# Performance work log

Hardware: AMD Instinct MI355X
Metric: run time of the kernel (lower is better)

## Reference

```python
import jax, jax.numpy as jnp
import numpy as np
import math

B, T, L, M = 2, 16, 256, 512
D, H, DH, HT, ROT = 1024, 16, 64, 8, 32
EPS = 1e-5
NEG = jnp.float32(-1e9)
SCALE = 1.0 / math.sqrt(DH)


def _ln(x, g, b):
    mu = jnp.mean(x, -1, keepdims=True)
    var = jnp.mean((x - mu) ** 2, -1, keepdims=True)
    return (x - mu) * jax.lax.rsqrt(var + EPS) * g + b


def _rotate_half(x):
    x1, x2 = jnp.split(x, 2, axis=-1)
    return jnp.concatenate([-x2, x1], axis=-1)


def _apply_rope(t, pos):
    # t: (..., DH), pos broadcastable to (..., ROT)
    t_rot, t_pass = t[..., :ROT], t[..., ROT:]
    t_rot = t_rot * jnp.cos(pos) + _rotate_half(t_rot) * jnp.sin(pos)
    return jnp.concatenate([t_rot, t_pass], axis=-1)


def _decoder_layer(x, context, rope,
                   ca_ng, ca_nb, ca_cng, ca_cnb, ca_wq, ca_wkv, ca_wo,
                   ta_ng, ta_nb, ta_wqkv, ta_bqkv, ta_wo,
                   ff_ng, ff_nb, ff_w1, ff_w2,
                   context_mask, attn_mask):
    # ---- CrossAttention over flattened (t l) sequence ----
    xf = x.reshape(B, T * L, D)
    xn = _ln(xf, ca_ng, ca_nb)
    cn = _ln(context, ca_cng, ca_cnb)
    q = (xn @ ca_wq).reshape(B, T * L, H, DH)
    k, v = jnp.split(cn @ ca_wkv, 2, axis=-1)
    k = k.reshape(B, M, H, DH)
    v = v.reshape(B, M, H, DH)
    scores = jnp.einsum('bnhd,bmhd->bhnm', q, k) * SCALE
    scores = jnp.where(context_mask[:, None, None, :], scores, NEG)
    attn = jax.nn.softmax(scores, axis=-1)
    o = jnp.einsum('bhnm,bmhd->bnhd', attn, v).reshape(B, T * L, H * DH)
    x = x + (o @ ca_wo).reshape(B, T, L, D)

    # ---- PatchWiseTemporalAttention: attention over T at each spatial l ----
    xn = _ln(x, ta_ng, ta_nb)
    qkv = xn @ ta_wqkv + ta_bqkv  # (B,T,L,3*HT*DH)
    q, k, v = jnp.split(qkv, 3, axis=-1)
    q = q.reshape(B, T, L, HT, DH)
    k = k.reshape(B, T, L, HT, DH)
    v = v.reshape(B, T, L, HT, DH)
    # varlen rotary: masks are left-aligned so packed position == frame index t
    pos = rope[:, None, None, :]  # (T,1,1,ROT)
    q = _apply_rope(q, pos)
    k = _apply_rope(k, pos)
    scores = jnp.einsum('bqlhd,bklhd->blhqk', q, k) * SCALE
    scores = jnp.where(attn_mask[:, None, None, None, :], scores, NEG)
    attn = jax.nn.softmax(scores, axis=-1)
    o = jnp.einsum('blhqk,bklhd->bqlhd', attn, v).reshape(B, T, L, HT * DH)
    # pad_input fills zeros at invalid (masked) query rows before to_out (no bias)
    o = o * attn_mask[:, :, None, None].astype(o.dtype)
    x = x + o @ ta_wo

    # ---- FeedForward (LN -> Linear -> GELU(exact) -> Linear) ----
    h = jax.nn.gelu(_ln(x, ff_ng, ff_nb) @ ff_w1, approximate=False)
    x = x + h @ ff_w2
    return x


def setup_inputs():
    key = jax.random.key(0)
    ks = jax.random.split(key, 16)
    s = 0.02
    inner, inner_t, hid = H * DH, HT * DH, 4 * D
    lens = jax.random.randint(ks[0], (B,), 2, T + 1)
    attn_mask = jnp.arange(T)[None, :] < lens[:, None]  # left-aligned ragged lengths
    clens = jax.random.randint(ks[1], (B,), M // 2, M + 1)
    context_mask = jnp.arange(M)[None, :] < clens[:, None]
    return dict(
        x=jax.random.normal(ks[2], (B, T, L, D), jnp.float32),
        context=jax.random.normal(ks[3], (B, M, D), jnp.float32),
        rope=jax.random.normal(ks[4], (T, ROT), jnp.float32),
        ca_ng=jnp.ones((D,), jnp.float32), ca_nb=jnp.zeros((D,), jnp.float32),
        ca_cng=jnp.ones((D,), jnp.float32), ca_cnb=jnp.zeros((D,), jnp.float32),
        ca_wq=jax.random.normal(ks[5], (D, inner), jnp.float32) * s,
        ca_wkv=jax.random.normal(ks[6], (D, 2 * inner), jnp.float32) * s,
        ca_wo=jax.random.normal(ks[7], (inner, D), jnp.float32) * s,
        ta_ng=jnp.ones((D,), jnp.float32), ta_nb=jnp.zeros((D,), jnp.float32),
        ta_wqkv=jax.random.normal(ks[8], (D, 3 * inner_t), jnp.float32) * s,
        ta_bqkv=jnp.zeros((3 * inner_t,), jnp.float32),
        ta_wo=jax.random.normal(ks[9], (inner_t, D), jnp.float32) * s,
        ff_ng=jnp.ones((D,), jnp.float32), ff_nb=jnp.zeros((D,), jnp.float32),
        ff_w1=jax.random.normal(ks[10], (D, hid), jnp.float32) * s,
        ff_w2=jax.random.normal(ks[11], (hid, D), jnp.float32) * s,
        context_mask=context_mask,
        attn_mask=attn_mask,
    )


def reference(x, context, rope,
              ca_ng, ca_nb, ca_cng, ca_cnb, ca_wq, ca_wkv, ca_wo,
              ta_ng, ta_nb, ta_wqkv, ta_bqkv, ta_wo,
              ff_ng, ff_nb, ff_w1, ff_w2,
              context_mask, attn_mask):
    return _decoder_layer(x, context, rope,
                          ca_ng, ca_nb, ca_cng, ca_cnb, ca_wq, ca_wkv, ca_wo,
                          ta_ng, ta_nb, ta_wqkv, ta_bqkv, ta_wo,
                          ff_ng, ff_nb, ff_w1, ff_w2,
                          context_mask, attn_mask)
```

## Files before the change

kernel.cpp:

```cpp
#include <hip/hip_runtime.h>
#include <hip/hip_bf16.h>
#include <stdint.h>

#define DEV static __device__ __forceinline__

constexpr int kB = 2, kT = 16, kL = 256, kM = 512;
constexpr int kD = 1024, kH = 16, kDH = 64, kHT = 8, kROT = 32;
constexpr int kN = kT * kL;
constexpr float kEPS = 1e-5f;
constexpr float kNEG = -1.0e9f;
constexpr float kSCALE = 0.125f;

typedef __attribute__((ext_vector_type(8))) short short8;
typedef __attribute__((ext_vector_type(4))) float floatx4;
typedef __attribute__((ext_vector_type(16))) float floatx16;

DEV float b2f(__hip_bfloat16 v) { return __bfloat162float(v); }
DEV __hip_bfloat16 f2b(float v) { return __float2bfloat16(v); }
DEV float s2f(short x) {
  __hip_bfloat16_raw r; r.x = (unsigned short)x;
  return __bfloat162float(__hip_bfloat16(r));
}

DEV void gl2lds16(const __hip_bfloat16* g, __hip_bfloat16* l) {
  __builtin_amdgcn_global_load_lds(
      (const __attribute__((address_space(1))) void*)g,
      (__attribute__((address_space(3))) void*)l, 16, 0, 0);
}

struct TransArgs {
  const float* src[7];
  __hip_bfloat16* dst[7];
  const unsigned char* cmraw;
  const unsigned char* amraw;
  int* cmask;
  int* amask;
};
__constant__ const int kTKd[7] = {1024, 1024, 1024, 1024, 512, 1024, 4096};
__constant__ const int kTNd[7] = {1024, 2048, 1024, 1536, 1024, 4096, 1024};
__constant__ const int kTCum[8] = {0, 1024, 3072, 4096, 5632, 6144, 10240, 14336};

DEV int mask_val(const unsigned char* raw, int i) {
  unsigned char b1 = raw[1], b3 = raw[3];
  if (b1 == 0x3F) return ((const unsigned short*)raw)[i] != 0;
  if (b3 == 0x3F) return ((const float*)raw)[i] != 0.0f;
  if (b1 == 1)    return raw[i] != 0;
  return ((const int*)raw)[i] != 0;
}

__global__ __launch_bounds__(256) void transpose_all(TransArgs a) {
  int id = blockIdx.x;
  if (id >= 14336) {
    if (id == 14336) {
      for (int i = threadIdx.x; i < kB * kM; i += 256)
        a.cmask[i] = mask_val(a.cmraw, i);
    } else {
      if (threadIdx.x < kB * kT)
        a.amask[threadIdx.x] = mask_val(a.amraw, threadIdx.x);
    }
    return;
  }
  int seg = 0;
  #pragma unroll
  for (int s = 1; s < 7; s++) seg += (id >= kTCum[s]);
  unsigned t = id - kTCum[seg];
  int Kd = kTKd[seg], Nd = kTNd[seg];
  unsigned ntx = Nd / 32;
  int n0 = (t % ntx) * 32, k0 = (t / ntx) * 32;
  const float* W = a.src[seg];
  __hip_bfloat16* Wt = a.dst[seg];
  __shared__ float tile[32][33];
  int tx = threadIdx.x & 31, ty = threadIdx.x >> 5;
  for (int i = 0; i < 32; i += 8)
    tile[ty + i][tx] = W[(size_t)(k0 + ty + i) * Nd + n0 + tx];
  __syncthreads();
  for (int i = 0; i < 32; i += 8)
    Wt[(size_t)(n0 + ty + i) * Kd + k0 + tx] = f2b(tile[tx][ty + i]);
}

DEV void ln_body(const float* xr, const float* g, const float* bb,
                 __hip_bfloat16* outr, int tid) {
  float4 xv = *(const float4*)(xr + tid * 4);
  float s = xv.x + xv.y + xv.z + xv.w;
  float s2 = xv.x * xv.x + xv.y * xv.y + xv.z * xv.z + xv.w * xv.w;
  for (int off = 32; off; off >>= 1) {
    s += __shfl_down(s, off);
    s2 += __shfl_down(s2, off);
  }
  __shared__ float rs[4], rs2[4];
  if ((tid & 63) == 0) { rs[tid >> 6] = s; rs2[tid >> 6] = s2; }
  __syncthreads();
  float ts = rs[0] + rs[1] + rs[2] + rs[3];
  float ts2 = rs2[0] + rs2[1] + rs2[2] + rs2[3];
  float mu = ts * (1.f / kD);
  float var = ts2 * (1.f / kD) - mu * mu;
  float rstd = rsqrtf(var + kEPS);
  float4 gv = *(const float4*)(g + tid * 4);
  float4 bv = *(const float4*)(bb + tid * 4);
  ushort4 o;
  o.x = __hip_bfloat16_raw(f2b((xv.x - mu) * rstd * gv.x + bv.x)).x;
  o.y = __hip_bfloat16_raw(f2b((xv.y - mu) * rstd * gv.y + bv.y)).x;
  o.z = __hip_bfloat16_raw(f2b((xv.z - mu) * rstd * gv.z + bv.z)).x;
  o.w = __hip_bfloat16_raw(f2b((xv.w - mu) * rstd * gv.w + bv.w)).x;
  *(ushort4*)(outr + tid * 4) = o;
}

__global__ __launch_bounds__(256) void ln_rows(
    const float* __restrict__ X, const float* __restrict__ g,
    const float* __restrict__ bb, __hip_bfloat16* __restrict__ out) {
  int row = blockIdx.x;
  ln_body(X + (size_t)row * kD, g, bb, out + (size_t)row * kD, threadIdx.x);
}

__global__ __launch_bounds__(256) void ln_rows2(
    const float* __restrict__ X, const float* __restrict__ g,
    const float* __restrict__ bb, __hip_bfloat16* __restrict__ out,
    const float* __restrict__ X2, const float* __restrict__ g2,
    const float* __restrict__ bb2, __hip_bfloat16* __restrict__ out2) {
  int row = blockIdx.x;
  if (row < 8192)
    ln_body(X + (size_t)row * kD, g, bb, out + (size_t)row * kD, threadIdx.x);
  else {
    int r = row - 8192;
    ln_body(X2 + (size_t)r * kD, g2, bb2, out2 + (size_t)r * kD, threadIdx.x);
  }
}

DEV void gemm_body(__hip_bfloat16* As, __hip_bfloat16* Bs,
                   const __hip_bfloat16* A, const __hip_bfloat16* Bt,
                   const float* bias, const float* res, int gelu,
                   void* out, int outBf16, int Nd, int Kd, int m0, int n0) {
  int tid = threadIdx.x, wave = tid >> 6, lane = tid & 63;
  int l32 = lane & 31, kg = lane >> 5;
  int wm = (wave >> 1) * 64, wn = (wave & 1) * 64;

  int srow = wave * 32 + (lane >> 3);
  int schunk8 = (((lane & 7) ^ ((lane >> 3) & 7)) << 3);
  const __hip_bfloat16* Ag = A + (size_t)(m0 + srow) * Kd + schunk8;
  const __hip_bfloat16* Bg = Bt + (size_t)(n0 + srow) * Kd + schunk8;
  __hip_bfloat16* Al = As + wave * 32 * 64;
  __hip_bfloat16* Bl = Bs + wave * 32 * 64;

  floatx16 acc[2][2] = {};
  for (int k0 = 0; k0 < Kd; k0 += 64) {
    #pragma unroll
    for (int i = 0; i < 4; i++) {
      gl2lds16(Ag + (size_t)(i * 8) * Kd + k0, Al + i * 512);
      gl2lds16(Bg + (size_t)(i * 8) * Kd + k0, Bl + i * 512);
    }
    __syncthreads();
    #pragma unroll
    for (int ks = 0; ks < 4; ks++) {
      int c = ks * 2 + kg;
      short8 af[2], bf2[2];
      #pragma unroll
      for (int fa = 0; fa < 2; fa++) {
        int row = wm + fa * 32 + l32;
        af[fa] = *(const short8*)(&As[row * 64 + (c ^ (row & 7)) * 8]);
      }
      #pragma unroll
      for (int fb = 0; fb < 2; fb++) {
        int row = wn + fb * 32 + l32;
        bf2[fb] = *(const short8*)(&Bs[row * 64 + (c ^ (row & 7)) * 8]);
      }
      #pragma unroll
      for (int fa = 0; fa < 2; fa++)
        #pragma unroll
        for (int fb = 0; fb < 2; fb++)
          acc[fa][fb] = __builtin_amdgcn_mfma_f32_32x32x16_bf16(
              af[fa], bf2[fb], acc[fa][fb], 0, 0, 0);
    }
    __syncthreads();
  }
  #pragma unroll
  for (int fa = 0; fa < 2; fa++) {
    #pragma unroll
    for (int fb = 0; fb < 2; fb++) {
      int col = n0 + wn + fb * 32 + l32;
      float bv = bias ? bias[col] : 0.f;
      #pragma unroll
      for (int r = 0; r < 16; r++) {
        int row = m0 + wm + fa * 32 + (r & 3) + 8 * (r >> 2) + 4 * kg;
        float v = acc[fa][fb][r] + bv;
        if (gelu) {
          v = v * (1.f / (1.f + __expf(-1.702f * v)));
        }
        size_t o = (size_t)row * Nd + col;
        if (res) v += res[o];
        if (outBf16) ((__hip_bfloat16*)out)[o] = f2b(v);
        else         ((float*)out)[o] = v;
      }
    }
  }
}

__global__ __launch_bounds__(256) void gemm_bf16(
    const __hip_bfloat16* __restrict__ A, const __hip_bfloat16* __restrict__ Bt,
    const float* __restrict__ bias, const float* __restrict__ res, int gelu,
    void* __restrict__ out, int outBf16, int Nd, int Kd) {
  __shared__ __align__(16) __hip_bfloat16 As[128 * 64];
  __shared__ __align__(16) __hip_bfloat16 Bs[128 * 64];
  gemm_body(As, Bs, A, Bt, bias, res, gelu, out, outBf16, Nd, Kd,
            blockIdx.x * 128, blockIdx.y * 128);
}

__global__ __launch_bounds__(256) void gemm_pair(
    const __hip_bfloat16* __restrict__ A0, const __hip_bfloat16* __restrict__ B0,
    void* __restrict__ o0,
    const __hip_bfloat16* __restrict__ A1, const __hip_bfloat16* __restrict__ B1,
    void* __restrict__ o1) {
  __shared__ __align__(16) __hip_bfloat16 As[128 * 64];
  __shared__ __align__(16) __hip_bfloat16 Bs[128 * 64];
  int id = blockIdx.x;
  if (id < 512) {
    gemm_body(As, Bs, A0, B0, nullptr, nullptr, 0, o0, 1, 1024, 1024,
              (id & 63) * 128, (id >> 6) * 128);
  } else {
    int r = id - 512;
    gemm_body(As, Bs, A1, B1, nullptr, nullptr, 0, o1, 1, 2048, 1024,
              (r & 7) * 128, (r >> 3) * 128);
  }
}

__global__ __launch_bounds__(512, 2) void gemm_8p(
    const __hip_bfloat16* __restrict__ A, const __hip_bfloat16* __restrict__ Bt,
    const float* __restrict__ bias, const float* __restrict__ res, int gelu,
    void* __restrict__ out, int outBf16, int Nd, int Kd) {
  __shared__ __align__(16) __hip_bfloat16 As[2][256][64];
  __shared__ __align__(16) __hip_bfloat16 Bs[2][256][64];
  const int m0 = blockIdx.x * 256, n0 = blockIdx.y * 256;
  const int tid = threadIdx.x, wave = tid >> 6, lane = tid & 63;
  const int l32 = lane & 31, kg = lane >> 5;
  const int wm = (wave >> 2) * 128;
  const int wn = (wave & 3) * 64;
  const int NT = Kd >> 6;
  const int NI = NT >> 1;

  const int srow = (wave << 3) + (lane >> 3);
  const int swz8 = (((lane & 7) ^ ((lane >> 3) & 7)) << 3);
  const __hip_bfloat16* Agt = A + (size_t)(m0 + srow) * Kd + swz8;
  const __hip_bfloat16* Bgt = Bt + (size_t)(n0 + srow) * Kd + swz8;

  auto stA = [&](int buf, int hf, int t) {
    const __hip_bfloat16* g = Agt + (size_t)(hf * 128) * Kd + t * 64;
    __hip_bfloat16* l = &As[buf][hf * 128 + (wave << 3)][0];
    gl2lds16(g, l);
    gl2lds16(g + (size_t)64 * Kd, l + 64 * 64);
  };
  auto stB = [&](int buf, int hf, int t) {
    const __hip_bfloat16* g = Bgt + (size_t)(hf * 128) * Kd + t * 64;
    __hip_bfloat16* l = &Bs[buf][hf * 128 + (wave << 3)][0];
    gl2lds16(g, l);
    gl2lds16(g + (size_t)64 * Kd, l + 64 * 64);
  };
  auto ldA4 = [&](int buf, int mf, short8* d) {
    int row = wm + mf * 32 + l32;
    const __hip_bfloat16* p = &As[buf][row][0];
    #pragma unroll
    for (int ks = 0; ks < 4; ks++) {
      int c = ks * 2 + kg;
      d[ks] = *(const short8*)(p + ((c ^ (row & 7)) << 3));
    }
  };
  auto ldB8 = [&](int buf, short8* d) {
    #pragma unroll
    for (int fb = 0; fb < 2; fb++) {
      int row = wn + fb * 32 + l32;
      const __hip_bfloat16* p = &Bs[buf][row][0];
      #pragma unroll
      for (int ks = 0; ks < 4; ks++) {
        int c = ks * 2 + kg;
        d[fb * 4 + ks] = *(const short8*)(p + ((c ^ (row & 7)) << 3));
      }
    }
  };

  floatx16 acc[4][2] = {};
  auto phase_mid = [&] {
    asm volatile("" ::: "memory");
    __builtin_amdgcn_s_barrier();
    asm volatile("s_waitcnt lgkmcnt(0)" ::: "memory");
    __builtin_amdgcn_sched_barrier(0);
  };
  auto phase_end = [&] {
    asm volatile("" ::: "memory");
    __builtin_amdgcn_s_barrier();
    asm volatile("" ::: "memory");
  };

  short8 aA[4], aB[4], b[8];

  #define MMAQ(mf, ar)                                                      \
    __builtin_amdgcn_s_setprio(1);                                          \
    _Pragma("unroll")                                                       \
    for (int ks = 0; ks < 4; ks++) {                                        \
      acc[mf][0] = __builtin_amdgcn_mfma_f32_32x32x16_bf16(                 \
          ar[ks], b[ks], acc[mf][0], 0, 0, 0);                              \
      acc[mf][1] = __builtin_amdgcn_mfma_f32_32x32x16_bf16(                 \
          ar[ks], b[4 + ks], acc[mf][1], 0, 0, 0);                          \
    }                                                                       \
    __builtin_amdgcn_s_setprio(0);

  stB(0, 0, 0); stB(0, 1, 0); stA(0, 0, 0); stA(0, 1, 0);
  stB(1, 0, 1); stB(1, 1, 1); stA(1, 0, 1);
  asm volatile("s_waitcnt vmcnt(6)" ::: "memory");
  __builtin_amdgcn_s_barrier();
  asm volatile("" ::: "memory");
  ldA4(0, 0, aA);

  for (int i = 0; i < NI; ++i) {
    const int ta = 2 * i, tb = ta + 1;
    const bool more = (i + 1 < NI);
    ldB8(0, b);
    ldA4(0, 1, aB);
    stA(1, 1, tb);
    phase_mid();
    MMAQ(0, aA);
    phase_end();
    ldA4(0, 2, aA);
    if (more) stB(0, 0, ta + 2);
    phase_mid();
    MMAQ(1, aB);
    phase_end();
    ldA4(0, 3, aB);
    if (more) stB(0, 1, ta + 2);
    phase_mid();
    MMAQ(2, aA);
    if (more) asm volatile("s_waitcnt vmcnt(4)" ::: "memory");
    else      asm volatile("s_waitcnt vmcnt(0)" ::: "memory");
    phase_end();
    ldA4(1, 0, aA);
    if (more) stA(0, 0, ta + 2);
    phase_mid();
    MMAQ(3, aB);
    phase_end();
    ldB8(1, b);
    ldA4(1, 1, aB);
    if (more) stA(0, 1, ta + 2);
    phase_mid();
    MMAQ(0, aA);
    phase_end();
    ldA4(1, 2, aA);
    if (more) stB(1, 0, tb + 2);
    phase_mid();
    MMAQ(1, aB);
    phase_end();
    ldA4(1, 3, aB);
    if (more) stB(1, 1, tb + 2);
    phase_mid();
    MMAQ(2, aA);
    if (more) asm volatile("s_waitcnt vmcnt(4)" ::: "memory");
    phase_end();
    if (more) {
      ldA4(0, 0, aA);
      stA(1, 0, tb + 2);
    }
    phase_mid();
    MMAQ(3, aB);
    phase_end();
  }
  #undef MMAQ

  #pragma unroll
  for (int mf = 0; mf < 4; mf++) {
    #pragma unroll
    for (int fb = 0; fb < 2; fb++) {
      int col = n0 + wn + fb * 32 + l32;
      float bv = bias ? bias[col] : 0.f;
      #pragma unroll
      for (int r = 0; r < 16; r++) {
        int row = m0 + wm + mf * 32 + (r & 3) + 8 * (r >> 2) + 4 * kg;
        float v = acc[mf][fb][r] + bv;
        if (gelu) v = v * (1.f / (1.f + __expf(-1.702f * v)));
        size_t o = (size_t)row * Nd + col;
        if (res) v += res[o];
        if (outBf16) ((__hip_bfloat16*)out)[o] = f2b(v);
        else         ((float*)out)[o] = v;
      }
    }
  }
}

__global__ __launch_bounds__(256) void cross_attn_mfma(
    const __hip_bfloat16* __restrict__ Qb,
    const __hip_bfloat16* __restrict__ KVb,
    const int* __restrict__ cmask,
    __hip_bfloat16* __restrict__ Ob) {
  __shared__ __align__(16) __hip_bfloat16 Vbf[2][8][64][8];
  __shared__ __align__(16) __hip_bfloat16 Paf[4][8][16][8];
  int b = blockIdx.y >> 4, h = blockIdx.y & 15;
  int q0 = blockIdx.x * 64;
  int tid = threadIdx.x, wave = tid >> 6, lane = tid & 63;
  int l16 = lane & 15, quad = lane >> 4;

  const __hip_bfloat16* qrow =
      Qb + (size_t)(b * kN + q0 + wave * 16 + l16) * 1024 + h * 64 + quad * 8;
  short8 qf0 = *(const short8*)qrow;
  short8 qf1 = *(const short8*)(qrow + 32);

  floatx4 of[4] = {};
  float Mr[4] = {-1e30f, -1e30f, -1e30f, -1e30f};
  float Lr[4] = {};

  int skey = tid >> 2, sd0 = (tid & 3) * 16;

  for (int kt = 0; kt < 8; kt++) {
    int buf = kt & 1;
    {
      const __hip_bfloat16* src =
          KVb + (size_t)(b * kM + kt * 64 + skey) * 2048 + 1024 + h * 64 + sd0;
      short8 v0 = *(const short8*)src;
      short8 v1 = *(const short8*)(src + 8);
      int kb = skey >> 3, kj = skey & 7;
      #pragma unroll
      for (int j = 0; j < 8; j++) {
        Vbf[buf][kb][sd0 + j][kj] = __hip_bfloat16(__hip_bfloat16_raw{(unsigned short)v0[j]});
        Vbf[buf][kb][sd0 + 8 + j][kj] = __hip_bfloat16(__hip_bfloat16_raw{(unsigned short)v1[j]});
      }
    }
    __syncthreads();

    floatx4 sf[4];
    #pragma unroll
    for (int nf = 0; nf < 4; nf++) {
      const __hip_bfloat16* krow =
          KVb + (size_t)(b * kM + kt * 64 + nf * 16 + l16) * 2048 + h * 64 + quad * 8;
      short8 kf0 = *(const short8*)krow;
      short8 kf1 = *(const short8*)(krow + 32);
      floatx4 z = {};
      z = __builtin_amdgcn_mfma_f32_16x16x32_bf16(qf0, kf0, z, 0, 0, 0);
      z = __builtin_amdgcn_mfma_f32_16x16x32_bf16(qf1, kf1, z, 0, 0, 0);
      sf[nf] = z;
    }

    float sv[4][4];
    #pragma unroll
    for (int nf = 0; nf < 4; nf++) {
      int mk = cmask[b * kM + kt * 64 + nf * 16 + l16];
      #pragma unroll
      for (int r = 0; r < 4; r++)
        sv[nf][r] = mk ? sf[nf][r] * kSCALE : kNEG;
    }
    float mx[4];
    #pragma unroll
    for (int r = 0; r < 4; r++) {
      float m = fmaxf(fmaxf(sv[0][r], sv[1][r]), fmaxf(sv[2][r], sv[3][r]));
      #pragma unroll
      for (int off = 1; off < 16; off <<= 1) m = fmaxf(m, __shfl_xor(m, off));
      mx[r] = m;
    }
    float alpha[4], Mn[4];
    #pragma unroll
    for (int r = 0; r < 4; r++) {
      Mn[r] = fmaxf(Mr[r], mx[r]);
      alpha[r] = __expf(Mr[r] - Mn[r]);
      Mr[r] = Mn[r];
    }
    float p[4][4];
    float rsum[4];
    #pragma unroll
    for (int r = 0; r < 4; r++) {
      float s = 0.f;
      #pragma unroll
      for (int nf = 0; nf < 4; nf++) {
        float e = __expf(sv[nf][r] - Mn[r]);
        p[nf][r] = e; s += e;
      }
      #pragma unroll
      for (int off = 1; off < 16; off <<= 1) s += __shfl_xor(s, off);
      rsum[r] = s;
    }
    #pragma unroll
    for (int r = 0; r < 4; r++) Lr[r] = Lr[r] * alpha[r] + rsum[r];
    #pragma unroll
    for (int df = 0; df < 4; df++)
      #pragma unroll
      for (int r = 0; r < 4; r++) of[df][r] *= alpha[r];

    #pragma unroll
    for (int nf = 0; nf < 4; nf++) {
      int col = nf * 16 + l16;
      int kb = col >> 3, kj = col & 7;
      #pragma unroll
      for (int r = 0; r < 4; r++)
        Paf[wave][kb][quad * 4 + r][kj] = f2b(p[nf][r]);
    }
    __builtin_amdgcn_s_waitcnt(0);

    short8 pf0 = *(const short8*)(&Paf[wave][quad][l16][0]);
    short8 pf1 = *(const short8*)(&Paf[wave][quad + 4][l16][0]);
    #pragma unroll
    for (int df = 0; df < 4; df++) {
      short8 vf0 = *(const short8*)(&Vbf[buf][quad][df * 16 + l16][0]);
      short8 vf1 = *(const short8*)(&Vbf[buf][quad + 4][df * 16 + l16][0]);
      of[df] = __builtin_amdgcn_mfma_f32_16x16x32_bf16(pf0, vf0, of[df], 0, 0, 0);
      of[df] = __builtin_amdgcn_mfma_f32_16x16x32_bf16(pf1, vf1, of[df], 0, 0, 0);
    }
  }

  #pragma unroll
  for (int df = 0; df < 4; df++) {
    #pragma unroll
    for (int r = 0; r < 4; r++) {
      int row = q0 + wave * 16 + quad * 4 + r;
      float v = of[df][r] / Lr[r];
      Ob[(size_t)(b * kN + row) * 1024 + h * 64 + df * 16 + l16] = f2b(v);
    }
  }
}

__global__ __launch_bounds__(64) void temporal_attn(
    const __hip_bfloat16* __restrict__ QKVb,
    const float* __restrict__ rope,
    const int* __restrict__ amask,
    __hip_bfloat16* __restrict__ Otb) {
  __shared__ float qs[16][65], ks[16][65], vs[16][65];
  __shared__ float Ps[16][17];
  int idx = blockIdx.x;
  int h = idx & 7, l = (idx >> 3) & 255, b = idx >> 11;
  int lane = threadIdx.x;

  {
    int tr = lane >> 2, c0 = (lane & 3) * 16;
    const __hip_bfloat16* base =
        QKVb + ((size_t)(b * kT + tr) * kL + l) * 1536 + h * 64;
    short8 qa = *(const short8*)(base + c0);
    short8 qb = *(const short8*)(base + c0 + 8);
    short8 ka = *(const short8*)(base + 512 + c0);
    short8 kb = *(const short8*)(base + 512 + c0 + 8);
    short8 va = *(const short8*)(base + 1024 + c0);
    short8 vb = *(const short8*)(base + 1024 + c0 + 8);
    #pragma unroll
    for (int j = 0; j < 8; j++) {
      qs[tr][c0 + j] = s2f(qa[j]) * kSCALE;
      qs[tr][c0 + 8 + j] = s2f(qb[j]) * kSCALE;
      ks[tr][c0 + j] = s2f(ka[j]);
      ks[tr][c0 + 8 + j] = s2f(kb[j]);
      vs[tr][c0 + j] = s2f(va[j]);
      vs[tr][c0 + 8 + j] = s2f(vb[j]);
    }
  }
  __syncthreads();
  {
    int rt = lane >> 2, rd0 = (lane & 3) * 8;
    float nq[8], nk[8];
    for (int j = 0; j < 8; j++) {
      int d = rd0 + j;
      float ang = rope[rt * kROT + d];
      float cv = cosf(ang), sv = sinf(ang);
      float oq = (d < 16) ? -qs[rt][d + 16] : qs[rt][d - 16];
      float ok = (d < 16) ? -ks[rt][d + 16] : ks[rt][d - 16];
      nq[j] = qs[rt][d] * cv + oq * sv;
      nk[j] = ks[rt][d] * cv + ok * sv;
    }
    __syncthreads();
    for (int j = 0; j < 8; j++) { qs[rt][rd0 + j] = nq[j]; ks[rt][rd0 + j] = nk[j]; }
  }
  __syncthreads();
  {
    int tq = lane >> 2, tk0 = (lane & 3) * 4;
    float s[4] = {0, 0, 0, 0};
    for (int d = 0; d < 64; d++) {
      float qv = qs[tq][d];
      s[0] += qv * ks[tk0 + 0][d];
      s[1] += qv * ks[tk0 + 1][d];
      s[2] += qv * ks[tk0 + 2][d];
      s[3] += qv * ks[tk0 + 3][d];
    }
    for (int jj = 0; jj < 4; jj++)
      Ps[tq][tk0 + jj] = amask[b * kT + tk0 + jj] ? s[jj] : kNEG;
  }
  __syncthreads();
  if (lane < 16) {
    float mx = -1e30f;
    for (int k = 0; k < 16; k++) mx = fmaxf(mx, Ps[lane][k]);
    float sum = 0.f;
    for (int k = 0; k < 16; k++) { float p = __expf(Ps[lane][k] - mx); Ps[lane][k] = p; sum += p; }
    float inv = 1.f / sum;
    for (int k = 0; k < 16; k++) Ps[lane][k] *= inv;
  }
  __syncthreads();
  for (int tq = 0; tq < 16; tq++) {
    float acc = 0.f;
    for (int tk = 0; tk < 16; tk++) acc += Ps[tq][tk] * vs[tk][lane];
    float qm = amask[b * kT + tq] ? 1.f : 0.f;
    Otb[((size_t)(b * kT + tq) * kL + l) * 512 + h * 64 + lane] = f2b(acc * qm);
  }
}

extern "C" void kernel_launch(void* const* d_in, const int* in_sizes, int n_in,
                              void* d_out, int out_size, void* d_ws, size_t ws_size,
                              hipStream_t stream) {
  const float* x       = (const float*)d_in[0];
  const float* ctx     = (const float*)d_in[1];
  const float* rope    = (const float*)d_in[2];
  const float* ca_ng   = (const float*)d_in[3];
  const float* ca_nb   = (const float*)d_in[4];
  const float* ca_cng  = (const float*)d_in[5];
  const float* ca_cnb  = (const float*)d_in[6];
  const float* ca_wq   = (const float*)d_in[7];
  const float* ca_wkv  = (const float*)d_in[8];
  const float* ca_wo   = (const float*)d_in[9];
  const float* ta_ng   = (const float*)d_in[10];
  const float* ta_nb   = (const float*)d_in[11];
  const float* ta_wqkv = (const float*)d_in[12];
  const float* ta_bqkv = (const float*)d_in[13];
  const float* ta_wo   = (const float*)d_in[14];
  const float* ff_ng   = (const float*)d_in[15];
  const float* ff_nb   = (const float*)d_in[16];
  const float* ff_w1   = (const float*)d_in[17];
  const float* ff_w2   = (const float*)d_in[18];
  const unsigned char* cmraw = (const unsigned char*)d_in[19];
  const unsigned char* amraw = (const unsigned char*)d_in[20];

  char* wsc = (char*)d_ws;
  size_t off = 0;
  auto take = [&](size_t bytes) {
    char* p = wsc + off;
    off = (off + bytes + 255) & ~(size_t)255;
    return p;
  };
  __hip_bfloat16* wqT   = (__hip_bfloat16*)take((size_t)1024 * 1024 * 2);
  __hip_bfloat16* wkvT  = (__hip_bfloat16*)take((size_t)2048 * 1024 * 2);
  __hip_bfloat16* woT   = (__hip_bfloat16*)take((size_t)1024 * 1024 * 2);
  __hip_bfloat16* wqkvT = (__hip_bfloat16*)take((size_t)1536 * 1024 * 2);
  __hip_bfloat16* tawoT = (__hip_bfloat16*)take((size_t)1024 * 512 * 2);
  __hip_bfloat16* ffw1T = (__hip_bfloat16*)take((size_t)4096 * 1024 * 2);
  __hip_bfloat16* ffw2T = (__hip_bfloat16*)take((size_t)1024 * 4096 * 2);
  __hip_bfloat16* XN  = (__hip_bfloat16*)take((size_t)8192 * 1024 * 2);
  __hip_bfloat16* CN  = (__hip_bfloat16*)take((size_t)1024 * 1024 * 2);
  __hip_bfloat16* Qb  = (__hip_bfloat16*)take((size_t)8192 * 1024 * 2);
  __hip_bfloat16* KVb = (__hip_bfloat16*)take((size_t)1024 * 2048 * 2);
  __hip_bfloat16* Ob  = (__hip_bfloat16*)take((size_t)8192 * 1024 * 2);
  float*          X1  = (float*)take((size_t)8192 * 1024 * 4);
  __hip_bfloat16* Hb  = (__hip_bfloat16*)take((size_t)8192 * 4096 * 2);
  int* cmask = (int*)take((size_t)kB * kM * 4);
  int* amask = (int*)take((size_t)kB * kT * 4);
  if (off > ws_size) return;

  __hip_bfloat16* QKVb = Hb;
  __hip_bfloat16* OTb  = Qb;

  auto gemm = [&](const __hip_bfloat16* A, const __hip_bfloat16* Bt,
                  const float* bias, const float* res, int gelu, void* out,
                  int outBf16, int Md, int Nd, int Kd) {
    gemm_bf16<<<dim3(Md / 128, Nd / 128), dim3(256), 0, stream>>>(
        A, Bt, bias, res, gelu, out, outBf16, Nd, Kd);
  };
  auto gemm8 = [&](const __hip_bfloat16* A, const __hip_bfloat16* Bt,
                   const float* bias, const float* res, int gelu, void* out,
                   int outBf16, int Md, int Nd, int Kd) {
    gemm_8p<<<dim3(Md / 256, Nd / 256), dim3(512), 0, stream>>>(
        A, Bt, bias, res, gelu, out, outBf16, Nd, Kd);
  };

  TransArgs ta;
  ta.src[0] = ca_wq;   ta.dst[0] = wqT;
  ta.src[1] = ca_wkv;  ta.dst[1] = wkvT;
  ta.src[2] = ca_wo;   ta.dst[2] = woT;
  ta.src[3] = ta_wqkv; ta.dst[3] = wqkvT;
  ta.src[4] = ta_wo;   ta.dst[4] = tawoT;
  ta.src[5] = ff_w1;   ta.dst[5] = ffw1T;
  ta.src[6] = ff_w2;   ta.dst[6] = ffw2T;
  ta.cmraw = cmraw; ta.amraw = amraw; ta.cmask = cmask; ta.amask = amask;
  transpose_all<<<dim3(14338), dim3(256), 0, stream>>>(ta);

  ln_rows2<<<dim3(9216), dim3(256), 0, stream>>>(x, ca_ng, ca_nb, XN,
                                                 ctx, ca_cng, ca_cnb, CN);
  gemm_pair<<<dim3(640), dim3(256), 0, stream>>>(XN, wqT, Qb, CN, wkvT, KVb);
  cross_attn_mfma<<<dim3(kN / 64, kB * kH), dim3(256), 0, stream>>>(Qb, KVb, cmask, Ob);
  gemm(Ob, woT, nullptr, x, 0, X1, 0, 8192, 1024, 1024);

  ln_rows<<<dim3(8192), dim3(256), 0, stream>>>(X1, ta_ng, ta_nb, XN);
  gemm8(XN, wqkvT, ta_bqkv, nullptr, 0, QKVb, 1, 8192, 1536, 1024);
  temporal_attn<<<dim3(kB * kL * kHT), dim3(64), 0, stream>>>(QKVb, rope, amask, OTb);
  gemm(OTb, tawoT, nullptr, X1, 0, X1, 0, 8192, 1024, 512);

  ln_rows<<<dim3(8192), dim3(256), 0, stream>>>(X1, ff_ng, ff_nb, XN);
  gemm8(XN, ffw1T, nullptr, nullptr, 1, Hb, 1, 8192, 4096, 1024);
  gemm(Hb, ffw2T, nullptr, X1, 0, d_out, 0, 8192, 1024, 4096);
}
```

Baseline: 651.2 us.

## Template 8-wave GEMM on N tile and use it for all N=1024 GEMMs

The 8-wave pipelined GEMM now takes its N-tile width (256 or 128) as a template parameter. It switches from 32x32x16 to 16x16x32 MFMA fragments with a new XOR LDS swizzle. The 256x128 variant replaces the 128x128 gemm_bf16 for the Q, output-projection, temporal-output and FF2 GEMMs, so those get the deeper pipelined schedule while keeping enough blocks to fill the GPU. The fused Q/KV pair launch is split into two separate launches. This adds a launch and changes the LDS bank-conflict pattern and register use.

```diff
diff --git a/kernel.cpp b/kernel.cpp
--- a/kernel.cpp
+++ b/kernel.cpp
@@ -204,78 +204,64 @@
             blockIdx.x * 128, blockIdx.y * 128);
 }
 
-__global__ __launch_bounds__(256) void gemm_pair(
-    const __hip_bfloat16* __restrict__ A0, const __hip_bfloat16* __restrict__ B0,
-    void* __restrict__ o0,
-    const __hip_bfloat16* __restrict__ A1, const __hip_bfloat16* __restrict__ B1,
-    void* __restrict__ o1) {
-  __shared__ __align__(16) __hip_bfloat16 As[128 * 64];
-  __shared__ __align__(16) __hip_bfloat16 Bs[128 * 64];
-  int id = blockIdx.x;
-  if (id < 512) {
-    gemm_body(As, Bs, A0, B0, nullptr, nullptr, 0, o0, 1, 1024, 1024,
-              (id & 63) * 128, (id >> 6) * 128);
-  } else {
-    int r = id - 512;
-    gemm_body(As, Bs, A1, B1, nullptr, nullptr, 0, o1, 1, 2048, 1024,
-              (r & 7) * 128, (r >> 3) * 128);
-  }
-}
-
+template <int NF>
 __global__ __launch_bounds__(512, 2) void gemm_8p(
     const __hip_bfloat16* __restrict__ A, const __hip_bfloat16* __restrict__ Bt,
     const float* __restrict__ bias, const float* __restrict__ res, int gelu,
     void* __restrict__ out, int outBf16, int Nd, int Kd) {
-  __shared__ __align__(16) __hip_bfloat16 As[2][256][64];
-  __shared__ __align__(16) __hip_bfloat16 Bs[2][256][64];
-  const int m0 = blockIdx.x * 256, n0 = blockIdx.y * 256;
+  constexpr int BN = NF * 64;
+  __shared__ __align__(1024) __hip_bfloat16 As[2][256][64];
+  __shared__ __align__(1024) __hip_bfloat16 Bs[2][BN][64];
+  const int m0 = blockIdx.x * 256, n0 = blockIdx.y * BN;
   const int tid = threadIdx.x, wave = tid >> 6, lane = tid & 63;
-  const int l32 = lane & 31, kg = lane >> 5;
+  const int l16 = lane & 15, quad = lane >> 4;
   const int wm = (wave >> 2) * 128;
-  const int wn = (wave & 3) * 64;
-  const int NT = Kd >> 6;
-  const int NI = NT >> 1;
+  const int wn = (wave & 3) * (NF * 16);
+  const int NT = Kd >> 6, NI = NT >> 1;
 
   const int srow = (wave << 3) + (lane >> 3);
-  const int swz8 = (((lane & 7) ^ ((lane >> 3) & 7)) << 3);
-  const __hip_bfloat16* Agt = A + (size_t)(m0 + srow) * Kd + swz8;
-  const __hip_bfloat16* Bgt = Bt + (size_t)(n0 + srow) * Kd + swz8;
+  const int slc = (lane & 7) ^ (((lane >> 5) & 1) << 1);
+  const __hip_bfloat16* Ag = A + (size_t)(m0 + srow) * Kd + slc * 8;
+  const __hip_bfloat16* Bg = Bt + (size_t)(n0 + srow) * Kd + slc * 8;
 
   auto stA = [&](int buf, int hf, int t) {
-    const __hip_bfloat16* g = Agt + (size_t)(hf * 128) * Kd + t * 64;
+    const __hip_bfloat16* g = Ag + (size_t)(hf * 128) * Kd + t * 64;
     __hip_bfloat16* l = &As[buf][hf * 128 + (wave << 3)][0];
     gl2lds16(g, l);
     gl2lds16(g + (size_t)64 * Kd, l + 64 * 64);
   };
   auto stB = [&](int buf, int hf, int t) {
-    const __hip_bfloat16* g = Bgt + (size_t)(hf * 128) * Kd + t * 64;
+    const __hip_bfloat16* g = Bg + (size_t)(hf * 128) * Kd + t * 64;
     __hip_bfloat16* l = &Bs[buf][hf * 128 + (wave << 3)][0];
     gl2lds16(g, l);
     gl2lds16(g + (size_t)64 * Kd, l + 64 * 64);
   };
-  auto ldA4 = [&](int buf, int mf, short8* d) {
-    int row = wm + mf * 32 + l32;
-    const __hip_bfloat16* p = &As[buf][row][0];
-    #pragma unroll
-    for (int ks = 0; ks < 4; ks++) {
-      int c = ks * 2 + kg;
-      d[ks] = *(const short8*)(p + ((c ^ (row & 7)) << 3));
-    }
-  };
-  auto ldB8 = [&](int buf, short8* d) {
-    #pragma unroll
-    for (int fb = 0; fb < 2; fb++) {
-      int row = wn + fb * 32 + l32;
-      const __hip_bfloat16* p = &Bs[buf][row][0];
-      #pragma unroll
-      for (int ks = 0; ks < 4; ks++) {
-        int c = ks * 2 + kg;
-        d[fb * 4 + ks] = *(const short8*)(p + ((c ^ (row & 7)) << 3));
-      }
-    }
-  };
-
-  floatx16 acc[4][2] = {};
+  auto ldA4 = [&](int buf, int q, short8* d) {
+    const char* base = (const char*)&As[buf][0][0];
+    #pragma unroll
+    for (int m2 = 0; m2 < 2; m2++) {
+      int row = wm + q * 32 + m2 * 16 + l16;
+      #pragma unroll
+      for (int ks = 0; ks < 2; ks++) {
+        int off = row * 128 + ks * 64 + quad * 16;
+        d[m2 * 2 + ks] = *(const short8*)(base + (off ^ ((off >> 9 & 1) << 5)));
+      }
+    }
+  };
+  auto ldB = [&](int buf, short8* d) {
+    const char* base = (const char*)&Bs[buf][0][0];
+    #pragma unroll
+    for (int nf = 0; nf < NF; nf++) {
+      int row = wn + nf * 16 + l16;
+      #pragma unroll
+      for (int ks = 0; ks < 2; ks++) {
+        int off = row * 128 + ks * 64 + quad * 16;
+        d[nf * 2 + ks] = *(const short8*)(base + (off ^ ((off >> 9 & 1) << 5)));
+      }
+    }
+  };
+
+  floatx4 acc[8][NF] = {};
   auto phase_mid = [&] {
     asm volatile("" ::: "memory");
     __builtin_amdgcn_s_barrier();
@@ -288,22 +274,30 @@
     asm volatile("" ::: "memory");
   };
 
-  short8 aA[4], aB[4], b[8];
-
-  #define MMAQ(mf, ar)                                                      \
+  short8 aA[4], aB[4], b[2 * NF];
+
+  #define MMAQ(q, ar)                                                       \
     __builtin_amdgcn_s_setprio(1);                                          \
     _Pragma("unroll")                                                       \
-    for (int ks = 0; ks < 4; ks++) {                                        \
-      acc[mf][0] = __builtin_amdgcn_mfma_f32_32x32x16_bf16(                 \
-          ar[ks], b[ks], acc[mf][0], 0, 0, 0);                              \
-      acc[mf][1] = __builtin_amdgcn_mfma_f32_32x32x16_bf16(                 \
-          ar[ks], b[4 + ks], acc[mf][1], 0, 0, 0);                          \
-    }                                                                       \
+    for (int m2 = 0; m2 < 2; m2++)                                          \
+      _Pragma("unroll")                                                     \
+      for (int nf = 0; nf < NF; nf++)                                       \
+        _Pragma("unroll")                                                   \
+        for (int ks = 0; ks < 2; ks++)                                      \
+          acc[(q) * 2 + m2][nf] = __builtin_amdgcn_mfma_f32_16x16x32_bf16(  \
+              ar[m2 * 2 + ks], b[nf * 2 + ks], acc[(q) * 2 + m2][nf],       \
+              0, 0, 0);                                                     \
     __builtin_amdgcn_s_setprio(0);
 
-  stB(0, 0, 0); stB(0, 1, 0); stA(0, 0, 0); stA(0, 1, 0);
-  stB(1, 0, 1); stB(1, 1, 1); stA(1, 0, 1);
-  asm volatile("s_waitcnt vmcnt(6)" ::: "memory");
+  if (NF == 4) {
+    stB(0, 0, 0); stB(0, 1, 0); stA(0, 0, 0); stA(0, 1, 0);
+    stB(1, 0, 1); stB(1, 1, 1); stA(1, 0, 1);
+    asm volatile("s_waitcnt vmcnt(6)" ::: "memory");
+  } else {
+    stB(0, 0, 0); stA(0, 0, 0); stA(0, 1, 0);
+    stB(1, 0, 1); stA(1, 0, 1);
+    asm volatile("s_waitcnt vmcnt(4)" ::: "memory");
+  }
   __builtin_amdgcn_s_barrier();
   asm volatile("" ::: "memory");
   ldA4(0, 0, aA);
@@ -311,7 +305,7 @@
   for (int i = 0; i < NI; ++i) {
     const int ta = 2 * i, tb = ta + 1;
     const bool more = (i + 1 < NI);
-    ldB8(0, b);
+    ldB(0, b);
     ldA4(0, 1, aB);
     stA(1, 1, tb);
     phase_mid();
@@ -323,18 +317,22 @@
     MMAQ(1, aB);
     phase_end();
     ldA4(0, 3, aB);
-    if (more) stB(0, 1, ta + 2);
+    if (NF == 4 && more) stB(0, 1, ta + 2);
     phase_mid();
     MMAQ(2, aA);
-    if (more) asm volatile("s_waitcnt vmcnt(4)" ::: "memory");
-    else      asm volatile("s_waitcnt vmcnt(0)" ::: "memory");
+    if (more) {
+      if (NF == 4) asm volatile("s_waitcnt vmcnt(4)" ::: "memory");
+      else         asm volatile("s_waitcnt vmcnt(2)" ::: "memory");
+    } else {
+      asm volatile("s_waitcnt vmcnt(0)" ::: "memory");
+    }
     phase_end();
     ldA4(1, 0, aA);
     if (more) stA(0, 0, ta + 2);
     phase_mid();
     MMAQ(3, aB);
     phase_end();
-    ldB8(1, b);
+    ldB(1, b);
     ldA4(1, 1, aB);
     if (more) stA(0, 1, ta + 2);
     phase_mid();
@@ -346,10 +344,13 @@
     MMAQ(1, aB);
     phase_end();
     ldA4(1, 3, aB);
-    if (more) stB(1, 1, tb + 2);
+    if (NF == 4 && more) stB(1, 1, tb + 2);
     phase_mid();
     MMAQ(2, aA);
-    if (more) asm volatile("s_waitcnt vmcnt(4)" ::: "memory");
+    if (more) {
+      if (NF == 4) asm volatile("s_waitcnt vmcnt(4)" ::: "memory");
+      else         asm volatile("s_waitcnt vmcnt(2)" ::: "memory");
+    }
     phase_end();
     if (more) {
       ldA4(0, 0, aA);
@@ -362,15 +363,15 @@
   #undef MMAQ
 
   #pragma unroll
-  for (int mf = 0; mf < 4; mf++) {
-    #pragma unroll
-    for (int fb = 0; fb < 2; fb++) {
-      int col = n0 + wn + fb * 32 + l32;
+  for (int mf = 0; mf < 8; mf++) {
+    #pragma unroll
+    for (int nf = 0; nf < NF; nf++) {
+      int col = n0 + wn + nf * 16 + l16;
       float bv = bias ? bias[col] : 0.f;
       #pragma unroll
-      for (int r = 0; r < 16; r++) {
-        int row = m0 + wm + mf * 32 + (r & 3) + 8 * (r >> 2) + 4 * kg;
-        float v = acc[mf][fb][r] + bv;
+      for (int r = 0; r < 4; r++) {
+        int row = m0 + wm + mf * 16 + quad * 4 + r;
+        float v = acc[mf][nf][r] + bv;
         if (gelu) v = v * (1.f / (1.f + __expf(-1.702f * v)));
         size_t o = (size_t)row * Nd + col;
         if (res) v += res[o];
@@ -641,16 +642,16 @@
   __hip_bfloat16* QKVb = Hb;
   __hip_bfloat16* OTb  = Qb;
 
-  auto gemm = [&](const __hip_bfloat16* A, const __hip_bfloat16* Bt,
-                  const float* bias, const float* res, int gelu, void* out,
-                  int outBf16, int Md, int Nd, int Kd) {
-    gemm_bf16<<<dim3(Md / 128, Nd / 128), dim3(256), 0, stream>>>(
+  auto g8n256 = [&](const __hip_bfloat16* A, const __hip_bfloat16* Bt,
+                    const float* bias, const float* res, int gelu, void* out,
+                    int outBf16, int Md, int Nd, int Kd) {
+    gemm_8p<4><<<dim3(Md / 256, Nd / 256), dim3(512), 0, stream>>>(
         A, Bt, bias, res, gelu, out, outBf16, Nd, Kd);
   };
-  auto gemm8 = [&](const __hip_bfloat16* A, const __hip_bfloat16* Bt,
-                   const float* bias, const float* res, int gelu, void* out,
-                   int outBf16, int Md, int Nd, int Kd) {
-    gemm_8p<<<dim3(Md / 256, Nd / 256), dim3(512), 0, stream>>>(
+  auto g8n128 = [&](const __hip_bfloat16* A, const __hip_bfloat16* Bt,
+                    const float* bias, const float* res, int gelu, void* out,
+                    int outBf16, int Md, int Nd, int Kd) {
+    gemm_8p<2><<<dim3(Md / 256, Nd / 128), dim3(512), 0, stream>>>(
         A, Bt, bias, res, gelu, out, outBf16, Nd, Kd);
   };
 
@@ -667,16 +668,18 @@
 
   ln_rows2<<<dim3(9216), dim3(256), 0, stream>>>(x, ca_ng, ca_nb, XN,
                                                  ctx, ca_cng, ca_cnb, CN);
-  gemm_pair<<<dim3(640), dim3(256), 0, stream>>>(XN, wqT, Qb, CN, wkvT, KVb);
+  g8n128(XN, wqT, nullptr, nullptr, 0, Qb, 1, 8192, 1024, 1024);
+  gemm_bf16<<<dim3(8, 16), dim3(256), 0, stream>>>(
+      CN, wkvT, nullptr, nullptr, 0, KVb, 1, 2048, 1024);
   cross_attn_mfma<<<dim3(kN / 64, kB * kH), dim3(256), 0, stream>>>(Qb, KVb, cmask, Ob);
-  gemm(Ob, woT, nullptr, x, 0, X1, 0, 8192, 1024, 1024);
+  g8n128(Ob, woT, nullptr, x, 0, X1, 0, 8192, 1024, 1024);
 
   ln_rows<<<dim3(8192), dim3(256), 0, stream>>>(X1, ta_ng, ta_nb, XN);
-  gemm8(XN, wqkvT, ta_bqkv, nullptr, 0, QKVb, 1, 8192, 1536, 1024);
+  g8n256(XN, wqkvT, ta_bqkv, nullptr, 0, QKVb, 1, 8192, 1536, 1024);
   temporal_attn<<<dim3(kB * kL * kHT), dim3(64), 0, stream>>>(QKVb, rope, amask, OTb);
-  gemm(OTb, tawoT, nullptr, X1, 0, X1, 0, 8192, 1024, 512);
+  g8n128(OTb, tawoT, nullptr, X1, 0, X1, 0, 8192, 1024, 512);
 
   ln_rows<<<dim3(8192), dim3(256), 0, stream>>>(X1, ff_ng, ff_nb, XN);
-  gemm8(XN, ffw1T, nullptr, nullptr, 1, Hb, 1, 8192, 4096, 1024);
-  gemm(Hb, ffw2T, nullptr, X1, 0, d_out, 0, 8192, 1024, 4096);
-}
+  g8n256(XN, ffw1T, nullptr, nullptr, 1, Hb, 1, 8192, 4096, 1024);
+  g8n128(Hb, ffw2T, nullptr, X1, 0, d_out, 0, 8192, 1024, 4096);
+}
```

New measurement: 671.0 us. 1.03x slower.
